# Optimization experiments

Hardware: AMD Instinct MI355X
Metric: run time of the kernel (lower is better)

The kernel has to match this reference:

```python
import jax, jax.numpy as jnp
import numpy as np

EMBED_DIM = 512
PATCH = 16
QUANT_N = 1024
QUANT_DIM = 256
LN_EPS = 1e-5


def setup_inputs() -> dict:
    key = jax.random.key(0)
    k1, k2, k3, k4 = jax.random.split(key, 4)
    B, T, M = 16, 8192, 128
    fbank = jax.random.normal(k1, (B, T, M), dtype=jnp.float32)
    # xavier-normal conv weight (O,I,kH,kW), frozen in the original module
    fan = PATCH * PATCH + EMBED_DIM
    conv_w = jax.random.normal(k2, (EMBED_DIM, 1, PATCH, PATCH), dtype=jnp.float32) * np.sqrt(2.0 / fan)
    proj = jax.random.normal(k3, (EMBED_DIM, QUANT_DIM), dtype=jnp.float32) * np.sqrt(2.0 / (EMBED_DIM + QUANT_DIM))
    codebook = jax.random.normal(k4, (QUANT_N, QUANT_DIM), dtype=jnp.float32)
    return {"fbank": fbank, "conv_w": conv_w, "proj": proj, "codebook": codebook}


def _l2norm(x, eps=1e-12):
    return x / jnp.maximum(jnp.linalg.norm(x, axis=-1, keepdims=True), eps)


def reference(fbank, conv_w, proj, codebook):
    # patch embedding: Conv2d(1, D, k=16, s=16) over (B, 1, T, mel)
    x = fbank[:, None, :, :]  # B,1,T,M
    feats = jax.lax.conv_general_dilated(
        x, conv_w, window_strides=(PATCH, PATCH), padding='VALID',
        dimension_numbers=('NCHW', 'OIHW', 'NCHW'))  # B,D,T/16,M/16
    B, D, H, W = feats.shape
    feats = feats.reshape(B, D, H * W).transpose(0, 2, 1)  # B,N,D
    # LayerNorm without affine
    mu = jnp.mean(feats, axis=-1, keepdims=True)
    var = jnp.var(feats, axis=-1, keepdims=True)
    feats = (feats - mu) * jax.lax.rsqrt(var + LN_EPS)
    # random projection quantizer: l2norm(x @ P) vs l2-normalized codebook;
    # argmin euclidean distance == argmax cosine similarity for unit vectors
    p = _l2norm(jnp.einsum('bnd,dq->bnq', feats, proj))  # B,N,Q
    cb = _l2norm(codebook)                                # K,Q
    sim = jnp.einsum('bnq,kq->bnk', p, cb)                # B,N,K
    embed_ind = jnp.argmax(sim, axis=-1)                  # B,N int
    return embed_ind
```

## Files before the change

### kernel.cpp

```cpp
#include <hip/hip_runtime.h>
#include <math.h>

#define QD 256
#define QN 1024
#define TT 8192

typedef __bf16 bf16x8 __attribute__((ext_vector_type(8)));
typedef float  f32x16 __attribute__((ext_vector_type(16)));
typedef unsigned short ushort_t;
typedef unsigned short us8 __attribute__((ext_vector_type(8)));

#define PL  0
#define MU_ 49152
#define LM_ 51200
#define TN_ 51328
#define LX_ 52352
#define TH_ 53376
#define CN_ 53504
#define CC_ 53632
#define SMEM_TOTAL 57728

__device__ __forceinline__ void split3(float x, ushort_t& h, ushort_t& m, ushort_t& l) {
    unsigned int xu = __float_as_uint(x);
    h = (ushort_t)(xu >> 16);
    float hf = __uint_as_float(xu & 0xFFFF0000u);
    float r1 = x - hf;
    unsigned int r1u = __float_as_uint(r1);
    m = (ushort_t)(r1u >> 16);
    float mf = __uint_as_float(r1u & 0xFFFF0000u);
    float r2 = r1 - mf;
    l = (ushort_t)(__float_as_uint(r2) >> 16);
}
__device__ __forceinline__ f32x16 MF(bf16x8 a, bf16x8 b, f32x16 c) {
    return __builtin_amdgcn_mfma_f32_32x32x16_bf16(a, b, c, 0, 0, 0);
}

__global__ __launch_bounds__(256) void k_pre(const float* __restrict__ convw,
                                             const float* __restrict__ proj,
                                             const float* __restrict__ cb,
                                             ushort_t* __restrict__ cbph,
                                             float* __restrict__ cbn,
                                             ushort_t* __restrict__ w2p,
                                             float* __restrict__ wsum,
                                             float* __restrict__ p1) {
    int bx = blockIdx.x, t = threadIdx.x;
    if (bx < 256) {
        int c = bx*4 + (t>>6), lane = t&63;
        float4 v = ((const float4*)(cb + (size_t)c*QD))[lane];
        float ss = v.x*v.x + v.y*v.y + v.z*v.z + v.w*v.w;
        #pragma unroll
        for (int off = 32; off > 0; off >>= 1) ss += __shfl_down(ss, off);
        ss = __shfl(ss, 0);
        float inv = 1.0f/fmaxf(sqrtf(ss), 1e-12f);
        float4 vn = make_float4(v.x*inv, v.y*inv, v.z*inv, v.w*inv);
        *(float4*)(cbn + (size_t)c*QD + 4*lane) = vn;
        float vals[4] = {vn.x, vn.y, vn.z, vn.w};
        #pragma unroll
        for (int i = 0; i < 4; ++i) {
            int k = 4*lane + i;
            size_t base = ((size_t)(k>>4)*32 + (c>>5))*512 + (((k>>3)&1)*32 + (c&31))*8 + (k&7);
            cbph[base] = (ushort_t)(__float_as_uint(vals[i]) >> 16);
        }
    } else {
        int col = bx - 256;
        __shared__ float colv[512];
        if (col < 256) {
            const float* src = proj + col;
            colv[t]       = src[(size_t)t * 256];
            colv[t + 256] = src[(size_t)(t + 256) * 256];
            __syncthreads();
            float acc = 0.f;
            #pragma unroll 32
            for (int d = 0; d < 512; ++d) acc += convw[d*256 + t] * colv[d];
            ushort_t hb, mb, lb; split3(acc, hb, mb, lb);
            size_t base = ((size_t)(t>>4)*8 + (col>>5))*512 + (((t>>3)&1)*32 + (col&31))*8 + (t&7);
            w2p[base] = hb;
            w2p[base + 65536] = mb;
            w2p[base + 131072] = lb;
        } else if (col == 256) {
            float s = 0.f;
            #pragma unroll 32
            for (int d = 0; d < 512; ++d) s += convw[d*256 + t];
            wsum[t] = s;
        } else {
            float s = 0.f;
            #pragma unroll 32
            for (int d = 0; d < 512; ++d) s += proj[d*256 + t];
            p1[t] = s;
        }
    }
}

__global__ __launch_bounds__(512, 4) void k_mega(const float* __restrict__ fbank,
                                                 const ushort_t* __restrict__ w2p,
                                                 const ushort_t* __restrict__ cbph,
                                                 const float* __restrict__ cbn,
                                                 const float* __restrict__ wsum,
                                                 const float* __restrict__ p1,
                                                 int* __restrict__ out) {
    __shared__ char smem[SMEM_TOTAL];
    float* muS   = (float*)(smem + MU_);
    float* lnMuS = (float*)(smem + LM_);
    float* tn2P  = (float*)(smem + TN_);
    float* lmaxS = (float*)(smem + LX_);
    float* thrS  = (float*)(smem + TH_);
    int*   cntS  = (int*)(smem + CN_);
    ushort_t* candS = (ushort_t*)(smem + CC_);

    int tid = threadIdx.x;
    int n0 = blockIdx.x * 32;
    int w = tid >> 6, lane = tid & 63;
    int n31 = lane & 31, h = lane >> 5;
    size_t loff = (size_t)lane * 16;
    const char* w2pc = (const char*)w2p;
    const char* cbhc = (const char*)cbph;

    auto loadB1 = [&](int kcv, bf16x8 (&dst)[3]) {
        #pragma unroll
        for (int q = 0; q < 3; ++q)
            dst[q] = *(const bf16x8*)(w2pc + (size_t)q*131072 + (size_t)(kcv*8 + w)*1024 + loff);
    };
    auto loadB2 = [&](int kcv, bf16x8 (&dst)[4]) {
        dst[0] = *(const bf16x8*)(cbhc + (size_t)(kcv*32 + w     )*1024 + loff);
        dst[1] = *(const bf16x8*)(cbhc + (size_t)(kcv*32 + w + 8 )*1024 + loff);
        dst[2] = *(const bf16x8*)(cbhc + (size_t)(kcv*32 + w + 16)*1024 + loff);
        dst[3] = *(const bf16x8*)(cbhc + (size_t)(kcv*32 + w + 24)*1024 + loff);
    };
    auto loadA = [&](int kcv, bf16x8 (&a)[3]) {
        #pragma unroll
        for (int p = 0; p < 3; ++p)
            a[p] = *(const bf16x8*)(smem + p*16384 + kcv*1024 + loff);
    };
    auto compute6 = [&](bf16x8 (&a)[3], bf16x8 (&b)[3], f32x16& acc) {
        acc = MF(a[0], b[0], acc);
        acc = MF(a[0], b[1], acc);
        acc = MF(a[1], b[0], acc);
        acc = MF(a[1], b[1], acc);
        acc = MF(a[0], b[2], acc);
        acc = MF(a[2], b[0], acc);
    };

    float4 va[2], vb[2];
    #pragma unroll
    for (int i = 0; i < 2; ++i) {
        int id = tid + 512*i;
        int kc = id >> 6, cl = id & 63;
        int tok = cl & 31, hh2 = cl >> 5;
        int n = n0 + tok;
        int b = n >> 12, r = n & 4095, th = r >> 3, wm = r & 7;
        const float* src = fbank + ((size_t)(b*TT + th*16 + kc))*128 + wm*16 + hh2*8;
        va[i] = ((const float4*)src)[0];
        vb[i] = ((const float4*)src)[1];
    }
    int kc0 = tid >> 6, hh0 = (tid >> 5) & 1;
    int wb0 = 16*kc0 + 8*hh0;
    float4 w00 = *(const float4*)(wsum + wb0);
    float4 w01 = *(const float4*)(wsum + wb0 + 4);
    float4 w10 = *(const float4*)(wsum + wb0 + 128);
    float4 w11 = *(const float4*)(wsum + wb0 + 132);
    float p1v = p1[32*w + n31];

    bf16x8 bA[3], bB[3];
    loadB1(0, bA);

    float wsv[2][8];
    wsv[0][0]=w00.x; wsv[0][1]=w00.y; wsv[0][2]=w00.z; wsv[0][3]=w00.w;
    wsv[0][4]=w01.x; wsv[0][5]=w01.y; wsv[0][6]=w01.z; wsv[0][7]=w01.w;
    wsv[1][0]=w10.x; wsv[1][1]=w10.y; wsv[1][2]=w10.z; wsv[1][3]=w10.w;
    wsv[1][4]=w11.x; wsv[1][5]=w11.y; wsv[1][6]=w11.z; wsv[1][7]=w11.w;

    float mupart = 0.f;
    #pragma unroll
    for (int i = 0; i < 2; ++i) {
        int id = tid + 512*i;
        int kc = id >> 6, cl = id & 63;
        float vals[8] = {va[i].x, va[i].y, va[i].z, va[i].w, vb[i].x, vb[i].y, vb[i].z, vb[i].w};
        us8 hv, mv, lv;
        #pragma unroll
        for (int j = 0; j < 8; ++j) {
            ushort_t a_, b_, c_; split3(vals[j], a_, b_, c_);
            hv[j] = a_; mv[j] = b_; lv[j] = c_;
            mupart += vals[j] * wsv[i][j];
        }
        char* cp = smem + kc*1024 + cl*16;
        *(us8*)cp = hv;
        *(us8*)(cp + 16384) = mv;
        *(us8*)(cp + 32768) = lv;
    }
    muS[(tid>>5)*32 + (tid&31)] = mupart;
    __syncthreads();

    if (tid < 32) {
        float pm = 0.f;
        #pragma unroll
        for (int s = 0; s < 16; ++s) pm += muS[s*32 + tid];
        lnMuS[tid] = pm * (1.f/512.f);
    }

    f32x16 accE, accO;
    #pragma unroll
    for (int r2 = 0; r2 < 16; ++r2) { accE[r2] = 0.f; accO[r2] = 0.f; }
    for (int kc = 0; kc < 16; kc += 2) {
        loadB1(kc + 1, bB);
        { bf16x8 a[3]; loadA(kc, a); compute6(a, bA, accE); }
        if (kc + 2 < 16) loadB1(kc + 2, bA);
        { bf16x8 a[3]; loadA(kc + 1, a); compute6(a, bB, accO); }
    }

    bf16x8 qA[4], qB[4];
    loadB2(0, qA);

    __syncthreads();

    {
        int q = 32*w + n31;
        #pragma unroll
        for (int reg = 0; reg < 16; ++reg) {
            int tok = (reg&3) + 8*(reg>>2) + 4*h;
            float tv = (accE[reg] + accO[reg]) - lnMuS[tok]*p1v;
            *(float*)(smem + 16384 + tok*1024 + q*4) = tv;
            *(ushort_t*)(smem + (q>>4)*1024 + (((q>>3)&1)*32 + tok)*16 + (q&7)*2)
                = (ushort_t)(__float_as_uint(tv) >> 16);
            float sq2 = tv*tv;
            #pragma unroll
            for (int msk = 1; msk < 32; msk <<= 1) sq2 += __shfl_xor(sq2, msk);
            if (n31 == 0) tn2P[tok*8 + w] = sq2;
        }
    }
    __syncthreads();

    f32x16 s0, s1, s2, s3;
    #pragma unroll
    for (int r2 = 0; r2 < 16; ++r2) { s0[r2]=0.f; s1[r2]=0.f; s2[r2]=0.f; s3[r2]=0.f; }
    for (int kc = 0; kc < 16; kc += 2) {
        loadB2(kc + 1, qB);
        {
            bf16x8 ah = *(const bf16x8*)(smem + kc*1024 + loff);
            s0 = MF(ah, qA[0], s0); s1 = MF(ah, qA[1], s1);
            s2 = MF(ah, qA[2], s2); s3 = MF(ah, qA[3], s3);
        }
        if (kc + 2 < 16) loadB2(kc + 2, qA);
        {
            bf16x8 ah = *(const bf16x8*)(smem + (kc+1)*1024 + loff);
            s0 = MF(ah, qB[0], s0); s1 = MF(ah, qB[1], s1);
            s2 = MF(ah, qB[2], s2); s3 = MF(ah, qB[3], s3);
        }
    }
    #pragma unroll
    for (int reg = 0; reg < 16; ++reg) {
        int tok = (reg&3) + 8*(reg>>2) + 4*h;
        float m = fmaxf(fmaxf(s0[reg], s1[reg]), fmaxf(s2[reg], s3[reg]));
        #pragma unroll
        for (int msk = 1; msk < 32; msk <<= 1) m = fmaxf(m, __shfl_xor(m, msk));
        if (n31 == 0) lmaxS[tok*8 + w] = m;
    }
    __syncthreads();
    if (tid < 32) {
        float g = -3.4e38f, sq = 0.f;
        #pragma unroll
        for (int p = 0; p < 8; ++p) { g = fmaxf(g, lmaxS[tid*8 + p]); sq += tn2P[tid*8 + p]; }
        thrS[tid] = g - 0.04f*sqrtf(sq);
        cntS[tid] = 0;
    }
    __syncthreads();
    #pragma unroll
    for (int reg = 0; reg < 16; ++reg) {
        int tok = (reg&3) + 8*(reg>>2) + 4*h;
        float th_ = thrS[tok];
        if (s0[reg] >= th_) { int p = atomicAdd(&cntS[tok], 1); if (p < 64) candS[tok*64 + p] = (ushort_t)(32*(w     ) + n31); }
        if (s1[reg] >= th_) { int p = atomicAdd(&cntS[tok], 1); if (p < 64) candS[tok*64 + p] = (ushort_t)(32*(w + 8 ) + n31); }
        if (s2[reg] >= th_) { int p = atomicAdd(&cntS[tok], 1); if (p < 64) candS[tok*64 + p] = (ushort_t)(32*(w + 16) + n31); }
        if (s3[reg] >= th_) { int p = atomicAdd(&cntS[tok], 1); if (p < 64) candS[tok*64 + p] = (ushort_t)(32*(w + 24) + n31); }
    }
    __syncthreads();
    #pragma unroll 1
    for (int tk = 0; tk < 4; ++tk) {
        int tok = 4*w + tk;
        float4 tv = *(const float4*)(smem + 16384 + tok*1024 + lane*16);
        int nc = cntS[tok];
        bool full = (nc > 64);
        if (full) nc = 1024;
        float bv = -3.4e38f; int bi = 0x7fffffff;
        int code = full ? 0 : candS[tok*64];
        float4 cv = *(const float4*)(cbn + (size_t)code*256 + 4*lane);
        for (int c = 0; c < nc; ++c) {
            int ncode = code;
            float4 nv = cv;
            if (c + 1 < nc) {
                ncode = full ? (c + 1) : (int)candS[tok*64 + c + 1];
                nv = *(const float4*)(cbn + (size_t)ncode*256 + 4*lane);
            }
            float d = cv.x*tv.x + cv.y*tv.y + cv.z*tv.z + cv.w*tv.w;
            #pragma unroll
            for (int msk = 1; msk < 64; msk <<= 1) d += __shfl_xor(d, msk);
            if (d > bv || (d == bv && code < bi)) { bv = d; bi = code; }
            code = ncode; cv = nv;
        }
        if (lane == 0) out[n0 + tok] = bi;
    }
}

extern "C" void kernel_launch(void* const* d_in, const int* in_sizes, int n_in,
                              void* d_out, int out_size, void* d_ws, size_t ws_size,
                              hipStream_t stream) {
    const float* fbank = (const float*)d_in[0];
    const float* convw = (const float*)d_in[1];
    const float* proj  = (const float*)d_in[2];
    const float* cbook = (const float*)d_in[3];
    int* out = (int*)d_out;

    char* ws = (char*)d_ws;
    ushort_t* cbph = (ushort_t*)ws;
    float* cbn     = (float*)(ws + 0x080000);
    ushort_t* w2p  = (ushort_t*)(ws + 0x180000);
    float* wsum    = (float*)(ws + 0x1E0000);
    float* p1      = (float*)(ws + 0x1E1000);

    hipLaunchKernelGGL(k_pre,  dim3(514),  dim3(256), 0, stream,
                       convw, proj, cbook, cbph, cbn, w2p, wsum, p1);
    hipLaunchKernelGGL(k_mega, dim3(2048), dim3(512), 0, stream,
                       fbank, w2p, cbph, cbn, wsum, p1, out);
}
```

Before: 316.5 us.

## Deepen B prefetch, merge threshold reductions via atomics, batch k_pre columns

```diff
diff --git a/kernel.cpp b/kernel.cpp
--- a/kernel.cpp
+++ b/kernel.cpp
@@ -13,12 +13,11 @@
 #define PL  0
 #define MU_ 49152
 #define LM_ 51200
-#define TN_ 51328
-#define LX_ 52352
-#define TH_ 53376
-#define CN_ 53504
-#define CC_ 53632
-#define SMEM_TOTAL 57728
+#define T2_ 51328
+#define TR_ 51456
+#define CN_ 51584
+#define CC_ 51712
+#define SMEM_TOTAL 55808
 
 __device__ __forceinline__ void split3(float x, ushort_t& h, ushort_t& m, ushort_t& l) {
     unsigned int xu = __float_as_uint(x);
@@ -33,6 +32,13 @@
 }
 __device__ __forceinline__ f32x16 MF(bf16x8 a, bf16x8 b, f32x16 c) {
     return __builtin_amdgcn_mfma_f32_32x32x16_bf16(a, b, c, 0, 0, 0);
+}
+__device__ __forceinline__ unsigned fenc(float f) {
+    unsigned u = __float_as_uint(f);
+    return (u & 0x80000000u) ? ~u : (u | 0x80000000u);
+}
+__device__ __forceinline__ float fdec(unsigned u) {
+    return (u & 0x80000000u) ? __uint_as_float(u ^ 0x80000000u) : __uint_as_float(~u);
 }
 
 __global__ __launch_bounds__(256) void k_pre(const float* __restrict__ convw,
@@ -61,50 +67,58 @@
             size_t base = ((size_t)(k>>4)*32 + (c>>5))*512 + (((k>>3)&1)*32 + (c&31))*8 + (k&7);
             cbph[base] = (ushort_t)(__float_as_uint(vals[i]) >> 16);
         }
-    } else {
-        int col = bx - 256;
-        __shared__ float colv[512];
-        if (col < 256) {
-            const float* src = proj + col;
-            colv[t]       = src[(size_t)t * 256];
-            colv[t + 256] = src[(size_t)(t + 256) * 256];
-            __syncthreads();
-            float acc = 0.f;
-            #pragma unroll 32
-            for (int d = 0; d < 512; ++d) acc += convw[d*256 + t] * colv[d];
-            ushort_t hb, mb, lb; split3(acc, hb, mb, lb);
+    } else if (bx < 320) {
+        int col0 = (bx - 256) * 4;
+        __shared__ float4 colv4[512];
+        const float* src = proj + col0;
+        colv4[t]       = *(const float4*)(src + (size_t)t * 256);
+        colv4[t + 256] = *(const float4*)(src + (size_t)(t + 256) * 256);
+        __syncthreads();
+        float a0 = 0.f, a1 = 0.f, a2 = 0.f, a3 = 0.f;
+        #pragma unroll 16
+        for (int d = 0; d < 512; ++d) {
+            float wv = convw[d*256 + t];
+            float4 cv = colv4[d];
+            a0 += wv*cv.x; a1 += wv*cv.y; a2 += wv*cv.z; a3 += wv*cv.w;
+        }
+        float accs[4] = {a0, a1, a2, a3};
+        #pragma unroll
+        for (int j = 0; j < 4; ++j) {
+            int col = col0 + j;
+            ushort_t hb, mb, lb; split3(accs[j], hb, mb, lb);
             size_t base = ((size_t)(t>>4)*8 + (col>>5))*512 + (((t>>3)&1)*32 + (col&31))*8 + (t&7);
             w2p[base] = hb;
             w2p[base + 65536] = mb;
             w2p[base + 131072] = lb;
-        } else if (col == 256) {
-            float s = 0.f;
-            #pragma unroll 32
-            for (int d = 0; d < 512; ++d) s += convw[d*256 + t];
-            wsum[t] = s;
-        } else {
-            float s = 0.f;
-            #pragma unroll 32
-            for (int d = 0; d < 512; ++d) s += proj[d*256 + t];
-            p1[t] = s;
-        }
-    }
-}
-
-__global__ __launch_bounds__(512, 4) void k_mega(const float* __restrict__ fbank,
-                                                 const ushort_t* __restrict__ w2p,
-                                                 const ushort_t* __restrict__ cbph,
-                                                 const float* __restrict__ cbn,
-                                                 const float* __restrict__ wsum,
-                                                 const float* __restrict__ p1,
-                                                 int* __restrict__ out) {
+        }
+    } else if (bx == 320) {
+        float s = 0.f;
+        #pragma unroll 32
+        for (int d = 0; d < 512; ++d) s += convw[d*256 + t];
+        wsum[t] = s;
+    } else {
+        float s = 0.f;
+        #pragma unroll 32
+        for (int d = 0; d < 512; ++d) s += proj[d*256 + t];
+        p1[t] = s;
+    }
+}
+
+__global__ __launch_bounds__(512)
+__attribute__((amdgpu_waves_per_eu(4, 4)))
+void k_mega(const float* __restrict__ fbank,
+            const ushort_t* __restrict__ w2p,
+            const ushort_t* __restrict__ cbph,
+            const float* __restrict__ cbn,
+            const float* __restrict__ wsum,
+            const float* __restrict__ p1,
+            int* __restrict__ out) {
     __shared__ char smem[SMEM_TOTAL];
-    float* muS   = (float*)(smem + MU_);
-    float* lnMuS = (float*)(smem + LM_);
-    float* tn2P  = (float*)(smem + TN_);
-    float* lmaxS = (float*)(smem + LX_);
-    float* thrS  = (float*)(smem + TH_);
-    int*   cntS  = (int*)(smem + CN_);
+    float*    muS   = (float*)(smem + MU_);
+    float*    lnMuS = (float*)(smem + LM_);
+    float*    tn2A  = (float*)(smem + T2_);
+    unsigned* thrR  = (unsigned*)(smem + TR_);
+    int*      cntS  = (int*)(smem + CN_);
     ushort_t* candS = (ushort_t*)(smem + CC_);
 
     int tid = threadIdx.x;
@@ -160,8 +174,11 @@
     float4 w11 = *(const float4*)(wsum + wb0 + 132);
     float p1v = p1[32*w + n31];
 
-    bf16x8 bA[3], bB[3];
-    loadB1(0, bA);
+    bf16x8 B1b[3][3];
+    loadB1(0, B1b[0]);
+    loadB1(1, B1b[1]);
+
+    if (tid < 32) { tn2A[tid] = 0.f; thrR[tid] = 0u; cntS[tid] = 0; }
 
     float wsv[2][8];
     wsv[0][0]=w00.x; wsv[0][1]=w00.y; wsv[0][2]=w00.z; wsv[0][3]=w00.w;
@@ -200,11 +217,12 @@
     f32x16 accE, accO;
     #pragma unroll
     for (int r2 = 0; r2 < 16; ++r2) { accE[r2] = 0.f; accO[r2] = 0.f; }
-    for (int kc = 0; kc < 16; kc += 2) {
-        loadB1(kc + 1, bB);
-        { bf16x8 a[3]; loadA(kc, a); compute6(a, bA, accE); }
-        if (kc + 2 < 16) loadB1(kc + 2, bA);
-        { bf16x8 a[3]; loadA(kc + 1, a); compute6(a, bB, accO); }
+    #pragma unroll
+    for (int kc = 0; kc < 16; ++kc) {
+        if (kc < 14) loadB1(kc + 2, B1b[(kc + 2) % 3]);
+        bf16x8 a[3]; loadA(kc, a);
+        if (kc & 1) compute6(a, B1b[kc % 3], accO);
+        else        compute6(a, B1b[kc % 3], accE);
     }
 
     bf16x8 qA[4], qB[4];
@@ -224,7 +242,7 @@
             float sq2 = tv*tv;
             #pragma unroll
             for (int msk = 1; msk < 32; msk <<= 1) sq2 += __shfl_xor(sq2, msk);
-            if (n31 == 0) tn2P[tok*8 + w] = sq2;
+            if (n31 == 0) atomicAdd(&tn2A[tok], sq2);
         }
     }
     __syncthreads();
@@ -252,27 +270,21 @@
         float m = fmaxf(fmaxf(s0[reg], s1[reg]), fmaxf(s2[reg], s3[reg]));
         #pragma unroll
         for (int msk = 1; msk < 32; msk <<= 1) m = fmaxf(m, __shfl_xor(m, msk));
-        if (n31 == 0) lmaxS[tok*8 + w] = m;
-    }
-    __syncthreads();
-    if (tid < 32) {
-        float g = -3.4e38f, sq = 0.f;
-        #pragma unroll
-        for (int p = 0; p < 8; ++p) { g = fmaxf(g, lmaxS[tid*8 + p]); sq += tn2P[tid*8 + p]; }
-        thrS[tid] = g - 0.04f*sqrtf(sq);
-        cntS[tid] = 0;
-    }
-    __syncthreads();
+        if (n31 == 0) atomicMax(&thrR[tok], fenc(m));
+    }
+    __syncthreads();
+
     #pragma unroll
     for (int reg = 0; reg < 16; ++reg) {
         int tok = (reg&3) + 8*(reg>>2) + 4*h;
-        float th_ = thrS[tok];
+        float th_ = fdec(thrR[tok]) - 0.04f*sqrtf(tn2A[tok]);
         if (s0[reg] >= th_) { int p = atomicAdd(&cntS[tok], 1); if (p < 64) candS[tok*64 + p] = (ushort_t)(32*(w     ) + n31); }
         if (s1[reg] >= th_) { int p = atomicAdd(&cntS[tok], 1); if (p < 64) candS[tok*64 + p] = (ushort_t)(32*(w + 8 ) + n31); }
         if (s2[reg] >= th_) { int p = atomicAdd(&cntS[tok], 1); if (p < 64) candS[tok*64 + p] = (ushort_t)(32*(w + 16) + n31); }
         if (s3[reg] >= th_) { int p = atomicAdd(&cntS[tok], 1); if (p < 64) candS[tok*64 + p] = (ushort_t)(32*(w + 24) + n31); }
     }
     __syncthreads();
+
     #pragma unroll 1
     for (int tk = 0; tk < 4; ++tk) {
         int tok = 4*w + tk;
@@ -281,20 +293,24 @@
         bool full = (nc > 64);
         if (full) nc = 1024;
         float bv = -3.4e38f; int bi = 0x7fffffff;
-        int code = full ? 0 : candS[tok*64];
-        float4 cv = *(const float4*)(cbn + (size_t)code*256 + 4*lane);
+        int c0 = full ? 0 : (int)candS[tok*64];
+        float4 v0 = *(const float4*)(cbn + (size_t)c0*256 + 4*lane);
+        int c1 = c0; float4 v1 = v0;
+        if (nc > 1) {
+            c1 = full ? 1 : (int)candS[tok*64 + 1];
+            v1 = *(const float4*)(cbn + (size_t)c1*256 + 4*lane);
+        }
         for (int c = 0; c < nc; ++c) {
-            int ncode = code;
-            float4 nv = cv;
-            if (c + 1 < nc) {
-                ncode = full ? (c + 1) : (int)candS[tok*64 + c + 1];
-                nv = *(const float4*)(cbn + (size_t)ncode*256 + 4*lane);
+            int c2 = c0; float4 v2 = v0;
+            if (c + 2 < nc) {
+                c2 = full ? (c + 2) : (int)candS[tok*64 + c + 2];
+                v2 = *(const float4*)(cbn + (size_t)c2*256 + 4*lane);
             }
-            float d = cv.x*tv.x + cv.y*tv.y + cv.z*tv.z + cv.w*tv.w;
+            float d = v0.x*tv.x + v0.y*tv.y + v0.z*tv.z + v0.w*tv.w;
             #pragma unroll
             for (int msk = 1; msk < 64; msk <<= 1) d += __shfl_xor(d, msk);
-            if (d > bv || (d == bv && code < bi)) { bv = d; bi = code; }
-            code = ncode; cv = nv;
+            if (d > bv || (d == bv && c0 < bi)) { bv = d; bi = c0; }
+            c0 = c1; v0 = v1; c1 = c2; v1 = v2;
         }
         if (lane == 0) out[n0 + tok] = bi;
     }
@@ -316,7 +332,7 @@
     float* wsum    = (float*)(ws + 0x1E0000);
     float* p1      = (float*)(ws + 0x1E1000);
 
-    hipLaunchKernelGGL(k_pre,  dim3(514),  dim3(256), 0, stream,
+    hipLaunchKernelGGL(k_pre,  dim3(322),  dim3(256), 0, stream,
                        convw, proj, cbook, cbph, cbn, w2p, wsum, p1);
     hipLaunchKernelGGL(k_mega, dim3(2048), dim3(512), 0, stream,
                        fbank, w2p, cbph, cbn, wsum, p1, out);
```

Result: slower. 328.4 us (+3.7%).
